# Optimization experiments

Hardware: AMD Instinct MI355X
Metric: run time of the kernel (lower is better)

The kernel has to match this reference:

```python
import jax, jax.numpy as jnp
import numpy as np

N = 50000          # nodes
E = 400000         # edges
MUL = 32           # multiplicity per irrep
NUM_NEIGHBORS = 8.0
INV_SQRT3 = 1.0 / np.sqrt(3.0)  # w3j(1,1,0) coefficient


def setup_inputs() -> dict:
    key = jax.random.key(0)
    ks = jax.random.split(key, 20)
    inp = {
        # node_input: 32x0e (dim 32) + 32x1o (dim 96) = 128
        "node_input": jax.random.normal(ks[0], (N, 4 * MUL), jnp.float32),
        "node_attr": jnp.ones((N, 1), jnp.float32),           # 1x0e trivial attr
        "edge_src": jax.random.randint(ks[1], (E,), 0, N, jnp.int32),
        "edge_dst": jax.random.randint(ks[2], (E,), 0, N, jnp.int32),
        "edge_attr": jax.random.normal(ks[3], (E, 4), jnp.float32),   # 1x0e + 1x1o
        "edge_scalars": jax.random.normal(ks[4], (E, 16), jnp.float32),
        # FullyConnectedTensorProduct weights (uvw, node_attr has mul 1)
        "w_sc0": jax.random.normal(ks[5], (MUL, MUL), jnp.float32),
        "w_sc1": jax.random.normal(ks[6], (MUL, MUL), jnp.float32),
        "w_lin1_0": jax.random.normal(ks[7], (MUL, MUL), jnp.float32),
        "w_lin1_1": jax.random.normal(ks[8], (MUL, MUL), jnp.float32),
        # radial FC net -> per-edge TP weights (numel = 4*MUL = 128)
        "fc_w1": jax.random.normal(ks[9], (16, 64), jnp.float32),
        "fc_w2": jax.random.normal(ks[10], (64, 4 * MUL), jnp.float32),
        # lin2: irreps_mid (64x0e+64x1o) x attr -> output
        "w_lin2_0": jax.random.normal(ks[11], (2 * MUL, MUL), jnp.float32),
        "w_lin2_1": jax.random.normal(ks[12], (2 * MUL, MUL), jnp.float32),
        # alpha: irreps_mid x attr -> 0e (zero-init in original; small randn for a nontrivial test)
        "w_alpha": 0.1 * jax.random.normal(ks[13], (2 * MUL, 1), jnp.float32),
        # sc_edges: irreps_mid x edge_attr -> edge_attr
        "w_se0a": jax.random.normal(ks[14], (2 * MUL,), jnp.float32),  # mid0e x ea0e -> 0e
        "w_se0b": jax.random.normal(ks[15], (2 * MUL,), jnp.float32),  # mid1o x ea1o -> 0e
        "w_se1a": jax.random.normal(ks[16], (2 * MUL,), jnp.float32),  # mid0e x ea1o -> 1o
        "w_se1b": jax.random.normal(ks[17], (2 * MUL,), jnp.float32),  # mid1o x ea0e -> 1o
    }
    return inp


def reference(node_input, node_attr, edge_src, edge_dst, edge_attr, edge_scalars,
              w_sc0, w_sc1, w_lin1_0, w_lin1_1, fc_w1, fc_w2,
              w_lin2_0, w_lin2_1, w_alpha, w_se0a, w_se0b, w_se1a, w_se1b):
    inv_nn = 1.0 / jnp.sqrt(jnp.asarray(NUM_NEIGHBORS, node_input.dtype))
    n = node_input.shape[0]
    x0 = node_input[:, :MUL]                       # (N, 32)   32x0e
    x1 = node_input[:, MUL:].reshape(n, MUL, 3)    # (N, 32, 3) 32x1o
    a = node_attr                                  # (N, 1)
    s_in = 1.0 / np.sqrt(MUL)                      # FCTP fan-in normalization

    # self-connection: FCTP(input, attr) -> output
    sc0 = (x0 @ w_sc0) * a * s_in
    sc1 = jnp.einsum('num,uw->nwm', x1, w_sc1) * a[:, :, None] * s_in
    node_self = jnp.concatenate([sc0, sc1.reshape(n, 3 * MUL)], axis=1)  # (N, 128)

    # lin1: FCTP(input, attr) -> input irreps
    f0 = (x0 @ w_lin1_0) * a * s_in
    f1 = jnp.einsum('num,uw->nwm', x1, w_lin1_1) * a[:, :, None] * s_in

    # gather source node features per edge
    g0 = f0[edge_src]                              # (E, 32)
    g1 = f1[edge_src]                              # (E, 32, 3)
    ea0 = edge_attr[:, :1]                         # (E, 1)   1x0e
    ea1 = edge_attr[:, 1:]                         # (E, 3)   1x1o

    # radial net -> per-edge TP weights (FullyConnectedNet with sin activation)
    h = jnp.sin(edge_scalars @ fc_w1 * (1.0 / np.sqrt(16.0)))
    w = h @ fc_w2 * (1.0 / np.sqrt(64.0))          # (E, 128)
    wA, wB, wC, wD = jnp.split(w, 4, axis=1)       # each (E, 32)

    # uvu tensor product, 4 instructions
    mA = wA * g0 * ea0                                           # 0e x 0e -> 0e
    mD = wD * jnp.einsum('eum,em->eu', g1, ea1) * INV_SQRT3      # 1o x 1o -> 0e
    mB = (wB * g0)[:, :, None] * ea1[:, None, :]                 # 0e x 1o -> 1o
    mC = (wC[:, :, None] * g1) * ea0[:, :, None]                 # 1o x 0e -> 1o
    mid0 = jnp.concatenate([mA, mD], axis=1)       # (E, 64)  64x0e
    mid1 = jnp.concatenate([mB, mC], axis=1)       # (E, 64, 3) 64x1o

    # scatter-add to destination nodes
    n0 = jax.ops.segment_sum(mid0, edge_dst, num_segments=n) * inv_nn
    n1 = jax.ops.segment_sum(mid1, edge_dst, num_segments=n) * inv_nn

    s_mid = 1.0 / np.sqrt(2 * MUL)
    out0 = (n0 @ w_lin2_0) * a * s_mid
    out1 = jnp.einsum('num,uw->nwm', n1, w_lin2_1) * a[:, :, None] * s_mid
    node_conv = jnp.concatenate([out0, out1.reshape(n, 3 * MUL)], axis=1)

    # alpha gate (sc.output_mask is all ones here, so alpha = 1 - 1 + alpha*1)
    alpha = (n0 @ w_alpha) * a * s_mid             # (N, 1)
    node_conv_out = node_self + alpha * node_conv  # (N, 128)

    # sc_edges: FCTP(mid, edge_attr) -> edge_attr irreps; fan-in = 128 per output
    s_se = 1.0 / np.sqrt(4 * MUL)
    se0 = ((mid0 @ w_se0a) * ea0[:, 0]
           + jnp.einsum('eum,em,u->e', mid1, ea1, w_se0b) * INV_SQRT3) * s_se
    se1 = ((mid0 @ w_se1a)[:, None] * ea1
           + jnp.einsum('eum,u->em', mid1, w_se1b) * ea0) * s_se
    edge_conv_out = edge_attr + jnp.concatenate([se0[:, None], se1], axis=1) * inv_nn

    return node_conv_out, edge_conv_out
```

## Files before the change

### kernel.cpp

```cpp
#include <hip/hip_runtime.h>
#include <math.h>

#define N_NODES 50000
#define E_EDGES 400000
#define NPRE_BLOCKS 6250
#define NHIST_BLOCKS 1563

typedef _Float16 f16x2 __attribute__((ext_vector_type(2)));
typedef _Float16 f16x4 __attribute__((ext_vector_type(4)));
typedef _Float16 f16x8 __attribute__((ext_vector_type(8)));
typedef float    f32x4 __attribute__((ext_vector_type(4)));

static constexpr float S_IN      = 0.17677669529663687f;
static constexpr float S_MID     = 0.125f;
static constexpr float S_SE      = 0.08838834764831843f;
static constexpr float INV_NN    = 0.35355339059327373f;
static constexpr float INV_SQRT3 = 0.5773502691896258f;
static constexpr float FC1_S     = 0.25f;
static constexpr float FC2_S     = 0.125f;

__device__ inline float wave_reduce_dpp(float v) {
    int x;
    x = __builtin_amdgcn_update_dpp(0, __float_as_int(v), 0x111, 0xf, 0xf, true); v += __int_as_float(x);
    x = __builtin_amdgcn_update_dpp(0, __float_as_int(v), 0x112, 0xf, 0xf, true); v += __int_as_float(x);
    x = __builtin_amdgcn_update_dpp(0, __float_as_int(v), 0x114, 0xf, 0xf, true); v += __int_as_float(x);
    x = __builtin_amdgcn_update_dpp(0, __float_as_int(v), 0x118, 0xf, 0xf, true); v += __int_as_float(x);
    x = __builtin_amdgcn_update_dpp(0, __float_as_int(v), 0x142, 0xa, 0xf, true); v += __int_as_float(x);
    x = __builtin_amdgcn_update_dpp(0, __float_as_int(v), 0x143, 0xc, 0xf, true); v += __int_as_float(x);
    return __int_as_float(__builtin_amdgcn_readlane(__float_as_int(v), 63));
}

__global__ __launch_bounds__(256) void pre_hist_kernel(
    const float* __restrict__ node_input, const float* __restrict__ node_attr,
    const float* __restrict__ w_sc0, const float* __restrict__ w_sc1,
    const float* __restrict__ w_lin1_0, const float* __restrict__ w_lin1_1,
    float* __restrict__ out_self, float* __restrict__ ws_f,
    const int* __restrict__ edge_dst, int* __restrict__ counts)
{
    const int t = threadIdx.x;
    if (blockIdx.x >= NPRE_BLOCKS) {
        const int e = (blockIdx.x - NPRE_BLOCKS) * 256 + t;
        if (e < E_EDGES) atomicAdd(&counts[edge_dst[e]], 1);
        return;
    }
    const int n0 = blockIdx.x * 8;
    __shared__ __align__(16) float sx[8 * 128];
    __shared__ float sa[8];
    ((float4*)sx)[t] = ((const float4*)(node_input + (size_t)n0 * 128))[t];
    if (t < 8) sa[t] = node_attr[n0 + t];
    __syncthreads();

    const int half = t >> 7;
    const int idx  = t & 127;
    float wcol[32];
    int m = 0;
    if (idx < 32) {
        const float* __restrict__ W = half ? w_lin1_0 : w_sc0;
        #pragma unroll
        for (int u = 0; u < 32; ++u) wcol[u] = W[u * 32 + idx];
    } else {
        const float* __restrict__ W = half ? w_lin1_1 : w_sc1;
        const int j = idx - 32;
        const int w = j / 3; m = j % 3;
        #pragma unroll
        for (int u = 0; u < 32; ++u) wcol[u] = W[u * 32 + w];
    }
    float* __restrict__ dstp = half ? ws_f : out_self;
    #pragma unroll
    for (int k = 0; k < 8; ++k) {
        const float* x = sx + k * 128;
        float acc = 0.f;
        if (idx < 32) {
            #pragma unroll
            for (int u = 0; u < 32; ++u) acc += x[u] * wcol[u];
        } else {
            #pragma unroll
            for (int u = 0; u < 32; ++u) acc += x[32 + u * 3 + m] * wcol[u];
        }
        dstp[(size_t)(n0 + k) * 128 + idx] = acc * sa[k] * S_IN;
    }
}

__global__ __launch_bounds__(1024) void scan_block_kernel(
    const int* __restrict__ counts, int* __restrict__ cursor, int* __restrict__ bsum)
{
    __shared__ int sd[1024];
    const int t   = threadIdx.x;
    const int idx = blockIdx.x * 1024 + t;
    const int c   = (idx < N_NODES) ? counts[idx] : 0;
    sd[t] = c;
    __syncthreads();
    for (int off = 1; off < 1024; off <<= 1) {
        const int v = (t >= off) ? sd[t - off] : 0;
        __syncthreads();
        sd[t] += v;
        __syncthreads();
    }
    if (idx < N_NODES) cursor[idx] = sd[t] - c;
    if (t == 1023) bsum[blockIdx.x] = sd[1023];
}

__global__ __launch_bounds__(1024) void scan_fixup_kernel(
    int* __restrict__ cursor, const int* __restrict__ bsum)
{
    __shared__ int boff_s;
    const int t = threadIdx.x;
    if (t < 64) {
        int v = (t < (int)blockIdx.x) ? bsum[t] : 0;
        #pragma unroll
        for (int off = 32; off >= 1; off >>= 1) v += __shfl_down(v, off, 64);
        if (t == 0) boff_s = v;
    }
    __syncthreads();
    const int idx = blockIdx.x * 1024 + t;
    if (idx < N_NODES) cursor[idx] += boff_s;
}

__global__ __launch_bounds__(256) void scatter_kernel(
    const int* __restrict__ edge_dst, int* __restrict__ cursor,
    int* __restrict__ sorted_eid)
{
    const int e = blockIdx.x * 256 + threadIdx.x;
    if (e < E_EDGES) {
        const int p = atomicAdd(&cursor[edge_dst[e]], 1);
        sorted_eid[p] = e;
    }
}

__global__ __launch_bounds__(256, 4) void edge_kernel(
    const float* __restrict__ ws_f,
    const int* __restrict__ edge_src, const int* __restrict__ edge_dst,
    const float* __restrict__ edge_attr, const float* __restrict__ edge_scalars,
    const float* __restrict__ fc_w1, const float* __restrict__ fc_w2,
    const float* __restrict__ w_se0a, const float* __restrict__ w_se0b,
    const float* __restrict__ w_se1a, const float* __restrict__ w_se1b,
    const int* __restrict__ sorted_eid,
    float* __restrict__ nacc, float* __restrict__ edge_out)
{
    __shared__ __align__(16) _Float16 sArena[18944];
    __shared__ __align__(16) float sEA[64 * 4];
    __shared__ __align__(16) float sDep[4][36];
    __shared__ int sSRC[64];
    __shared__ int sDST[64];
    __shared__ int sEID[64];

    _Float16* __restrict__ sW2T  = sArena;
    _Float16* __restrict__ sHT   = sArena + 9216;
    _Float16* __restrict__ sES   = sArena + 13824;
    _Float16* __restrict__ sW1T  = sArena + 16384;
    _Float16* __restrict__ sWt   = sArena;
    _Float16* __restrict__ sMidA = sArena + 8704;
    _Float16* __restrict__ sBT   = sArena + 12928;

    const int t    = threadIdx.x;
    const int lane = t & 63;
    const int wv   = t >> 6;
    const int quad = lane >> 4;
    const int mm   = lane & 15;
    const int e0   = blockIdx.x * 64;

    {
        const int k = t >> 4, n4 = (t & 15) * 4;
        float4 v = ((const float4*)fc_w1)[t];
        sW1T[(n4 + 0) * 40 + k] = (_Float16)v.x;
        sW1T[(n4 + 1) * 40 + k] = (_Float16)v.y;
        sW1T[(n4 + 2) * 40 + k] = (_Float16)v.z;
        sW1T[(n4 + 3) * 40 + k] = (_Float16)v.w;
        const f16x4 z4 = {(_Float16)0.f, (_Float16)0.f, (_Float16)0.f, (_Float16)0.f};
        *(f16x4*)&sW1T[(t >> 2) * 40 + 16 + (t & 3) * 4] = z4;
    }
    #pragma unroll
    for (int i = 0; i < 8; ++i) {
        const int u = t + i * 256;
        const int k = u >> 5, c4 = (u & 31) * 4;
        float4 v = ((const float4*)fc_w2)[u];
        sW2T[(c4 + 0) * 72 + k] = (_Float16)v.x;
        sW2T[(c4 + 1) * 72 + k] = (_Float16)v.y;
        sW2T[(c4 + 2) * 72 + k] = (_Float16)v.z;
        sW2T[(c4 + 3) * 72 + k] = (_Float16)v.w;
    }
    {
        const int e = t >> 2, k4 = (t & 3) * 4;
        const int eid = sorted_eid[e0 + e];
        float4 v = ((const float4*)edge_scalars)[(size_t)eid * 4 + (t & 3)];
        f16x4 p = {(_Float16)v.x, (_Float16)v.y, (_Float16)v.z, (_Float16)v.w};
        *(f16x4*)&sES[e * 40 + k4] = p;
        const f16x4 z4 = {(_Float16)0.f, (_Float16)0.f, (_Float16)0.f, (_Float16)0.f};
        *(f16x4*)&sES[e * 40 + 16 + k4] = z4;
    }
    if (t < 64) {
        const int eid = sorted_eid[e0 + t];
        *(float4*)&sEA[t * 4] = ((const float4*)edge_attr)[eid];
        sEID[t] = eid;
    } else if (t < 128) {
        sSRC[t - 64] = edge_src[sorted_eid[e0 + (t - 64)]];
    } else if (t < 192) {
        sDST[t - 128] = edge_dst[sorted_eid[e0 + (t - 128)]];
    }
    __syncthreads();

    const int eb = wv * 16;

    {
        const f16x8 b_es = *(const f16x8*)&sES[(eb + mm) * 40 + quad * 8];
        #pragma unroll
        for (int jt = 0; jt < 4; ++jt) {
            const f16x8 a_w1 = *(const f16x8*)&sW1T[(jt * 16 + mm) * 40 + quad * 8];
            f32x4 d = {0.f, 0.f, 0.f, 0.f};
            d = __builtin_amdgcn_mfma_f32_16x16x32_f16(a_w1, b_es, d, 0, 0, 0);
            f16x4 hv;
            hv[0] = (_Float16)__sinf(d[0] * FC1_S);
            hv[1] = (_Float16)__sinf(d[1] * FC1_S);
            hv[2] = (_Float16)__sinf(d[2] * FC1_S);
            hv[3] = (_Float16)__sinf(d[3] * FC1_S);
            *(f16x4*)&sHT[(eb + mm) * 72 + jt * 16 + quad * 4] = hv;
        }
    }
    __syncthreads();

    f32x4 dacc[8];
    {
        const f16x8 b_lo = *(const f16x8*)&sHT[(eb + mm) * 72 + quad * 8];
        const f16x8 b_hi = *(const f16x8*)&sHT[(eb + mm) * 72 + 32 + quad * 8];
        #pragma unroll
        for (int ct = 0; ct < 8; ++ct) {
            const f16x8 a_lo = *(const f16x8*)&sW2T[(ct * 16 + mm) * 72 + quad * 8];
            const f16x8 a_hi = *(const f16x8*)&sW2T[(ct * 16 + mm) * 72 + 32 + quad * 8];
            f32x4 d = {0.f, 0.f, 0.f, 0.f};
            d = __builtin_amdgcn_mfma_f32_16x16x32_f16(a_lo, b_lo, d, 0, 0, 0);
            d = __builtin_amdgcn_mfma_f32_16x16x32_f16(a_hi, b_hi, d, 0, 0, 0);
            dacc[ct] = d;
        }
    }
    __syncthreads();

    {
        #pragma unroll
        for (int ct = 0; ct < 8; ++ct) {
            f16x4 v;
            v[0] = (_Float16)(dacc[ct][0] * FC2_S);
            v[1] = (_Float16)(dacc[ct][1] * FC2_S);
            v[2] = (_Float16)(dacc[ct][2] * FC2_S);
            v[3] = (_Float16)(dacc[ct][3] * FC2_S);
            *(f16x4*)&sWt[(eb + mm) * 136 + ct * 16 + quad * 4] = v;
        }
        const f16x8 z8 = {};
        for (int i = t; i < 528; i += 256) *(f16x8*)&sBT[i * 8] = z8;
    }
    __syncthreads();
    {
        const int u = t & 63, p = t >> 6;
        const float ev = (p == 0) ? w_se0a[u] : w_se1b[u];
        const float ov = (p == 0) ? w_se1a[u] : w_se0b[u];
        sBT[(2 * p) * 264 + 4 * u + p]     = (_Float16)ev;
        sBT[(2 * p + 1) * 264 + 4 * u + p] = (_Float16)ov;
    }
    __syncthreads();

    const bool hi = lane >= 32;
    const int  u  = lane - 32;
    const int idxA = hi ? (32 + 3 * u) : lane;
    const int idxB = hi ? (33 + 3 * u) : lane;
    const int idxC = hi ? (34 + 3 * u) : lane;
    const int col1 = hi ? (96 + u) : lane;
    const int col2 = hi ? (64 + u) : (32 + lane);

    int   cur = -1;
    float am0 = 0.f, axx = 0.f, ayy = 0.f, azz = 0.f;
    _Float16* __restrict__ myA = sMidA + wv * 1056;
    const _Float16* __restrict__ arow = myA + (mm & 3) * 264;
    const _Float16* __restrict__ brow = sBT + mm * 264;

    for (int b = 0; b < 4; ++b) {
        float ga[4], gb[4], gc[4];
        #pragma unroll
        for (int i = 0; i < 4; ++i) {
            const int el = eb + b * 4 + i;
            const float* fr = ws_f + (size_t)sSRC[el] * 128;
            ga[i] = fr[idxA]; gb[i] = fr[idxB]; gc[i] = fr[idxC];
        }
        #pragma unroll
        for (int i = 0; i < 4; ++i) {
            const int el  = eb + b * 4 + i;
            const int dst = sDST[el];
            const float ea0 = sEA[el * 4 + 0];
            const float e1x = sEA[el * 4 + 1];
            const float e1y = sEA[el * 4 + 2];
            const float e1z = sEA[el * 4 + 3];
            const float w1v = (float)sWt[el * 136 + col1];
            const float w2v = (float)sWt[el * 136 + col2];

            float mid0, m1x, m1y, m1z;
            if (!hi) {
                mid0 = w1v * ga[i] * ea0;
                const float wbg = w2v * ga[i];
                m1x = wbg * e1x; m1y = wbg * e1y; m1z = wbg * e1z;
            } else {
                const float dot = ga[i] * e1x + gb[i] * e1y + gc[i] * e1z;
                mid0 = w1v * dot * INV_SQRT3;
                const float wce = w2v * ea0;
                m1x = wce * ga[i]; m1y = wce * gb[i]; m1z = wce * gc[i];
            }

            if (dst != cur) {
                if (cur >= 0) {
                    float* np_ = nacc + (size_t)cur * 256;
                    atomicAdd(np_ + lane, am0);
                    atomicAdd(np_ + 64 + lane * 3 + 0, axx);
                    atomicAdd(np_ + 64 + lane * 3 + 1, ayy);
                    atomicAdd(np_ + 64 + lane * 3 + 2, azz);
                }
                cur = dst; am0 = axx = ayy = azz = 0.f;
            }
            am0 += mid0; axx += m1x; ayy += m1y; azz += m1z;

            f16x4 mv;
            mv[0] = (_Float16)mid0; mv[1] = (_Float16)m1x;
            mv[2] = (_Float16)m1y;  mv[3] = (_Float16)m1z;
            *(f16x4*)&myA[i * 264 + 4 * lane] = mv;
        }

        f32x4 d = {0.f, 0.f, 0.f, 0.f};
        #pragma unroll
        for (int ks = 0; ks < 8; ++ks) {
            const f16x8 a  = *(const f16x8*)&arow[ks * 32 + quad * 8];
            const f16x8 bb = *(const f16x8*)&brow[ks * 32 + quad * 8];
            d = __builtin_amdgcn_mfma_f32_16x16x32_f16(a, bb, d, 0, 0, 0);
        }
        if (lane < 8) {
            float4 f4; f4.x = d[0]; f4.y = d[1]; f4.z = d[2]; f4.w = d[3];
            *(float4*)&sDep[wv][lane * 4] = f4;
        }
        if (lane < 4) {
            const int el = eb + b * 4 + lane;
            const float c0 = sDep[wv][ 0 + lane], c1 = sDep[wv][ 4 + lane];
            const float c2 = sDep[wv][ 8 + lane], c3 = sDep[wv][12 + lane];
            const float c4 = sDep[wv][16 + lane], c5 = sDep[wv][20 + lane];
            const float c6 = sDep[wv][24 + lane], c7 = sDep[wv][28 + lane];
            const float ea0 = sEA[el * 4 + 0];
            const float e1x = sEA[el * 4 + 1];
            const float e1y = sEA[el * 4 + 2];
            const float e1z = sEA[el * 4 + 3];
            const float s0 = c0 * ea0 + (c3 * e1x + c5 * e1y + c7 * e1z) * INV_SQRT3;
            float4 o;
            o.x = ea0 + s0 * S_SE * INV_NN;
            o.y = e1x + (c1 * e1x + c2 * ea0) * S_SE * INV_NN;
            o.z = e1y + (c1 * e1y + c4 * ea0) * S_SE * INV_NN;
            o.w = e1z + (c1 * e1z + c6 * ea0) * S_SE * INV_NN;
            *(float4*)&edge_out[(size_t)sEID[el] * 4] = o;
        }
    }
    if (cur >= 0) {
        float* np_ = nacc + (size_t)cur * 256;
        atomicAdd(np_ + lane, am0);
        atomicAdd(np_ + 64 + lane * 3 + 0, axx);
        atomicAdd(np_ + 64 + lane * 3 + 1, ayy);
        atomicAdd(np_ + 64 + lane * 3 + 2, azz);
    }
}

__global__ __launch_bounds__(128) void node_post_kernel(
    const float* __restrict__ nacc, const float* __restrict__ node_attr,
    const float* __restrict__ w_lin2_0, const float* __restrict__ w_lin2_1,
    const float* __restrict__ w_alpha, float* __restrict__ out)
{
    const int n0 = blockIdx.x * 8, t = threadIdx.x;
    __shared__ __align__(16) float sn[8 * 256];
    __shared__ float salpha[8];
    const float4* src = (const float4*)(nacc + (size_t)n0 * 256);
    #pragma unroll
    for (int i = 0; i < 4; ++i) ((float4*)sn)[t + i * 128] = src[t + i * 128];
    __syncthreads();

    if (t < 64) {
        const float wa = w_alpha[t];
        #pragma unroll
        for (int k = 0; k < 8; ++k) {
            const float r = wave_reduce_dpp(sn[k * 256 + t] * wa);
            if (t == 0) salpha[k] = r;
        }
    }
    __syncthreads();

    float wcol[64];
    int m = 0;
    if (t < 32) {
        #pragma unroll
        for (int u = 0; u < 64; ++u) wcol[u] = w_lin2_0[u * 32 + t];
    } else {
        const int j = t - 32; const int w = j / 3; m = j % 3;
        #pragma unroll
        for (int u = 0; u < 64; ++u) wcol[u] = w_lin2_1[u * 32 + w];
    }
    #pragma unroll
    for (int k = 0; k < 8; ++k) {
        const float* s = sn + k * 256;
        float acc = 0.f;
        if (t < 32) {
            #pragma unroll
            for (int u = 0; u < 64; ++u) acc += s[u] * wcol[u];
        } else {
            #pragma unroll
            for (int u = 0; u < 64; ++u) acc += s[64 + u * 3 + m] * wcol[u];
        }
        const float a  = node_attr[n0 + k];
        const float sc = a * S_MID * INV_NN;
        const size_t o = (size_t)(n0 + k) * 128 + t;
        out[o] = out[o] + (salpha[k] * sc) * (acc * sc);
    }
}

extern "C" void kernel_launch(void* const* d_in, const int* in_sizes, int n_in,
                              void* d_out, int out_size, void* d_ws, size_t ws_size,
                              hipStream_t stream)
{
    const float* node_input   = (const float*)d_in[0];
    const float* node_attr    = (const float*)d_in[1];
    const int*   edge_src     = (const int*)d_in[2];
    const int*   edge_dst     = (const int*)d_in[3];
    const float* edge_attr    = (const float*)d_in[4];
    const float* edge_scalars = (const float*)d_in[5];
    const float* w_sc0        = (const float*)d_in[6];
    const float* w_sc1        = (const float*)d_in[7];
    const float* w_lin1_0     = (const float*)d_in[8];
    const float* w_lin1_1     = (const float*)d_in[9];
    const float* fc_w1        = (const float*)d_in[10];
    const float* fc_w2        = (const float*)d_in[11];
    const float* w_lin2_0     = (const float*)d_in[12];
    const float* w_lin2_1     = (const float*)d_in[13];
    const float* w_alpha      = (const float*)d_in[14];
    const float* w_se0a       = (const float*)d_in[15];
    const float* w_se0b       = (const float*)d_in[16];
    const float* w_se1a       = (const float*)d_in[17];
    const float* w_se1b       = (const float*)d_in[18];

    float* out      = (float*)d_out;
    float* edge_out = out + (size_t)N_NODES * 128;

    float* ws_f   = (float*)d_ws;
    float* nacc   = ws_f + (size_t)N_NODES * 128;
    int*   counts = (int*)(nacc + (size_t)N_NODES * 256);
    int*   cursor = counts + N_NODES;
    int*   sid    = cursor + N_NODES;
    int*   bsum   = sid + E_EDGES;

    hipMemsetAsync(nacc, 0,
        ((size_t)N_NODES * 256 + N_NODES) * sizeof(float), stream);

    pre_hist_kernel<<<NPRE_BLOCKS + NHIST_BLOCKS, 256, 0, stream>>>(
        node_input, node_attr, w_sc0, w_sc1, w_lin1_0, w_lin1_1, out, ws_f,
        edge_dst, counts);

    scan_block_kernel<<<49, 1024, 0, stream>>>(counts, cursor, bsum);
    scan_fixup_kernel<<<49, 1024, 0, stream>>>(cursor, bsum);
    scatter_kernel<<<(E_EDGES + 255) / 256, 256, 0, stream>>>(edge_dst, cursor, sid);

    edge_kernel<<<E_EDGES / 64, 256, 0, stream>>>(
        ws_f, edge_src, edge_dst, edge_attr, edge_scalars, fc_w1, fc_w2,
        w_se0a, w_se0b, w_se1a, w_se1b, sid, nacc, edge_out);

    node_post_kernel<<<N_NODES / 8, 128, 0, stream>>>(
        nacc, node_attr, w_lin2_0, w_lin2_1, w_alpha, out);
}
```

Before: 414.3 us.

## Load FC1 operands into registers, prefetch gathers early, shrink LDS for occupancy

Result: no change. 420.9 us (+1.6%).

```diff
diff --git a/kernel.cpp b/kernel.cpp
--- a/kernel.cpp
+++ b/kernel.cpp
@@ -18,6 +18,8 @@
 static constexpr float INV_SQRT3 = 0.5773502691896258f;
 static constexpr float FC1_S     = 0.25f;
 static constexpr float FC2_S     = 0.125f;
+
+#define BAR_LDS() asm volatile("s_waitcnt lgkmcnt(0)\n\ts_barrier" ::: "memory")
 
 __device__ inline float wave_reduce_dpp(float v) {
     int x;
@@ -127,7 +129,7 @@
     }
 }
 
-__global__ __launch_bounds__(256, 4) void edge_kernel(
+__global__ __launch_bounds__(256, 5) void edge_kernel(
     const float* __restrict__ ws_f,
     const int* __restrict__ edge_src, const int* __restrict__ edge_dst,
     const float* __restrict__ edge_attr, const float* __restrict__ edge_scalars,
@@ -137,7 +139,7 @@
     const int* __restrict__ sorted_eid,
     float* __restrict__ nacc, float* __restrict__ edge_out)
 {
-    __shared__ __align__(16) _Float16 sArena[18944];
+    __shared__ __align__(16) _Float16 sArena[15040];
     __shared__ __align__(16) float sEA[64 * 4];
     __shared__ __align__(16) float sDep[4][36];
     __shared__ int sSRC[64];
@@ -146,8 +148,6 @@
 
     _Float16* __restrict__ sW2T  = sArena;
     _Float16* __restrict__ sHT   = sArena + 9216;
-    _Float16* __restrict__ sES   = sArena + 13824;
-    _Float16* __restrict__ sW1T  = sArena + 16384;
     _Float16* __restrict__ sWt   = sArena;
     _Float16* __restrict__ sMidA = sArena + 8704;
     _Float16* __restrict__ sBT   = sArena + 12928;
@@ -158,17 +158,31 @@
     const int quad = lane >> 4;
     const int mm   = lane & 15;
     const int e0   = blockIdx.x * 64;
-
-    {
-        const int k = t >> 4, n4 = (t & 15) * 4;
-        float4 v = ((const float4*)fc_w1)[t];
-        sW1T[(n4 + 0) * 40 + k] = (_Float16)v.x;
-        sW1T[(n4 + 1) * 40 + k] = (_Float16)v.y;
-        sW1T[(n4 + 2) * 40 + k] = (_Float16)v.z;
-        sW1T[(n4 + 3) * 40 + k] = (_Float16)v.w;
-        const f16x4 z4 = {(_Float16)0.f, (_Float16)0.f, (_Float16)0.f, (_Float16)0.f};
-        *(f16x4*)&sW1T[(t >> 2) * 40 + 16 + (t & 3) * 4] = z4;
-    }
+    const int eb   = wv * 16;
+
+    f16x8 a_w1[4];
+    f16x8 b_es = {};
+    if (quad < 2) {
+        const int myeid = sorted_eid[e0 + eb + mm];
+        const float4* esp = (const float4*)edge_scalars + (size_t)myeid * 4 + quad * 2;
+        const float4 v0 = esp[0];
+        const float4 v1 = esp[1];
+        b_es[0] = (_Float16)v0.x; b_es[1] = (_Float16)v0.y;
+        b_es[2] = (_Float16)v0.z; b_es[3] = (_Float16)v0.w;
+        b_es[4] = (_Float16)v1.x; b_es[5] = (_Float16)v1.y;
+        b_es[6] = (_Float16)v1.z; b_es[7] = (_Float16)v1.w;
+        const float* wb = fc_w1 + (quad << 3) * 64 + mm;
+        #pragma unroll
+        for (int jt = 0; jt < 4; ++jt) {
+            #pragma unroll
+            for (int s = 0; s < 8; ++s)
+                a_w1[jt][s] = (_Float16)wb[s * 64 + jt * 16];
+        }
+    } else {
+        #pragma unroll
+        for (int jt = 0; jt < 4; ++jt) a_w1[jt] = (f16x8){};
+    }
+
     #pragma unroll
     for (int i = 0; i < 8; ++i) {
         const int u = t + i * 256;
@@ -179,15 +193,6 @@
         sW2T[(c4 + 2) * 72 + k] = (_Float16)v.z;
         sW2T[(c4 + 3) * 72 + k] = (_Float16)v.w;
     }
-    {
-        const int e = t >> 2, k4 = (t & 3) * 4;
-        const int eid = sorted_eid[e0 + e];
-        float4 v = ((const float4*)edge_scalars)[(size_t)eid * 4 + (t & 3)];
-        f16x4 p = {(_Float16)v.x, (_Float16)v.y, (_Float16)v.z, (_Float16)v.w};
-        *(f16x4*)&sES[e * 40 + k4] = p;
-        const f16x4 z4 = {(_Float16)0.f, (_Float16)0.f, (_Float16)0.f, (_Float16)0.f};
-        *(f16x4*)&sES[e * 40 + 16 + k4] = z4;
-    }
     if (t < 64) {
         const int eid = sorted_eid[e0 + t];
         *(float4*)&sEA[t * 4] = ((const float4*)edge_attr)[eid];
@@ -197,26 +202,35 @@
     } else if (t < 192) {
         sDST[t - 128] = edge_dst[sorted_eid[e0 + (t - 128)]];
     }
-    __syncthreads();
-
-    const int eb = wv * 16;
-
-    {
-        const f16x8 b_es = *(const f16x8*)&sES[(eb + mm) * 40 + quad * 8];
-        #pragma unroll
-        for (int jt = 0; jt < 4; ++jt) {
-            const f16x8 a_w1 = *(const f16x8*)&sW1T[(jt * 16 + mm) * 40 + quad * 8];
-            f32x4 d = {0.f, 0.f, 0.f, 0.f};
-            d = __builtin_amdgcn_mfma_f32_16x16x32_f16(a_w1, b_es, d, 0, 0, 0);
-            f16x4 hv;
-            hv[0] = (_Float16)__sinf(d[0] * FC1_S);
-            hv[1] = (_Float16)__sinf(d[1] * FC1_S);
-            hv[2] = (_Float16)__sinf(d[2] * FC1_S);
-            hv[3] = (_Float16)__sinf(d[3] * FC1_S);
-            *(f16x4*)&sHT[(eb + mm) * 72 + jt * 16 + quad * 4] = hv;
-        }
-    }
-    __syncthreads();
+    BAR_LDS();
+
+    const bool hi = lane >= 32;
+    const int  u  = lane - 32;
+    const int idxA = hi ? (32 + 3 * u) : lane;
+    const int idxB = hi ? (33 + 3 * u) : lane;
+    const int idxC = hi ? (34 + 3 * u) : lane;
+    const int col1 = hi ? (96 + u) : lane;
+    const int col2 = hi ? (64 + u) : (32 + lane);
+
+    float ga[4][4], gb[4][4], gc[4][4];
+    #pragma unroll
+    for (int i = 0; i < 4; ++i) {
+        const float* fr = ws_f + (size_t)sSRC[eb + i] * 128;
+        ga[0][i] = fr[idxA]; gb[0][i] = fr[idxB]; gc[0][i] = fr[idxC];
+    }
+
+    #pragma unroll
+    for (int jt = 0; jt < 4; ++jt) {
+        f32x4 d = {0.f, 0.f, 0.f, 0.f};
+        d = __builtin_amdgcn_mfma_f32_16x16x32_f16(a_w1[jt], b_es, d, 0, 0, 0);
+        f16x4 hv;
+        hv[0] = (_Float16)__sinf(d[0] * FC1_S);
+        hv[1] = (_Float16)__sinf(d[1] * FC1_S);
+        hv[2] = (_Float16)__sinf(d[2] * FC1_S);
+        hv[3] = (_Float16)__sinf(d[3] * FC1_S);
+        *(f16x4*)&sHT[(eb + mm) * 72 + jt * 16 + quad * 4] = hv;
+    }
+    BAR_LDS();
 
     f32x4 dacc[8];
     {
@@ -232,7 +246,7 @@
             dacc[ct] = d;
         }
     }
-    __syncthreads();
+    BAR_LDS();
 
     {
         #pragma unroll
@@ -245,39 +259,32 @@
             *(f16x4*)&sWt[(eb + mm) * 136 + ct * 16 + quad * 4] = v;
         }
         const f16x8 z8 = {};
-        for (int i = t; i < 528; i += 256) *(f16x8*)&sBT[i * 8] = z8;
-    }
-    __syncthreads();
+        for (int i = t; i < 264; i += 256) *(f16x8*)&sBT[i * 8] = z8;
+    }
+    BAR_LDS();
     {
-        const int u = t & 63, p = t >> 6;
-        const float ev = (p == 0) ? w_se0a[u] : w_se1b[u];
-        const float ov = (p == 0) ? w_se1a[u] : w_se0b[u];
-        sBT[(2 * p) * 264 + 4 * u + p]     = (_Float16)ev;
-        sBT[(2 * p + 1) * 264 + 4 * u + p] = (_Float16)ov;
-    }
-    __syncthreads();
-
-    const bool hi = lane >= 32;
-    const int  u  = lane - 32;
-    const int idxA = hi ? (32 + 3 * u) : lane;
-    const int idxB = hi ? (33 + 3 * u) : lane;
-    const int idxC = hi ? (34 + 3 * u) : lane;
-    const int col1 = hi ? (96 + u) : lane;
-    const int col2 = hi ? (64 + u) : (32 + lane);
+        const int uu = t & 63, p = t >> 6;
+        const float ev = (p == 0) ? w_se0a[uu] : w_se1b[uu];
+        const float ov = (p == 0) ? w_se1a[uu] : w_se0b[uu];
+        sBT[(2 * p) * 264 + 4 * uu + p]     = (_Float16)ev;
+        sBT[(2 * p + 1) * 264 + 4 * uu + p] = (_Float16)ov;
+    }
+    BAR_LDS();
 
     int   cur = -1;
     float am0 = 0.f, axx = 0.f, ayy = 0.f, azz = 0.f;
     _Float16* __restrict__ myA = sMidA + wv * 1056;
     const _Float16* __restrict__ arow = myA + (mm & 3) * 264;
-    const _Float16* __restrict__ brow = sBT + mm * 264;
-
+    const _Float16* __restrict__ brow = sBT + (mm & 7) * 264;
+
+    #pragma unroll
     for (int b = 0; b < 4; ++b) {
-        float ga[4], gb[4], gc[4];
-        #pragma unroll
-        for (int i = 0; i < 4; ++i) {
-            const int el = eb + b * 4 + i;
-            const float* fr = ws_f + (size_t)sSRC[el] * 128;
-            ga[i] = fr[idxA]; gb[i] = fr[idxB]; gc[i] = fr[idxC];
+        if (b < 3) {
+            #pragma unroll
+            for (int i = 0; i < 4; ++i) {
+                const float* fr = ws_f + (size_t)sSRC[eb + (b + 1) * 4 + i] * 128;
+                ga[b + 1][i] = fr[idxA]; gb[b + 1][i] = fr[idxB]; gc[b + 1][i] = fr[idxC];
+            }
         }
         #pragma unroll
         for (int i = 0; i < 4; ++i) {
@@ -292,14 +299,14 @@
 
             float mid0, m1x, m1y, m1z;
             if (!hi) {
-                mid0 = w1v * ga[i] * ea0;
-                const float wbg = w2v * ga[i];
+                mid0 = w1v * ga[b][i] * ea0;
+                const float wbg = w2v * ga[b][i];
                 m1x = wbg * e1x; m1y = wbg * e1y; m1z = wbg * e1z;
             } else {
-                const float dot = ga[i] * e1x + gb[i] * e1y + gc[i] * e1z;
+                const float dot = ga[b][i] * e1x + gb[b][i] * e1y + gc[b][i] * e1z;
                 mid0 = w1v * dot * INV_SQRT3;
                 const float wce = w2v * ea0;
-                m1x = wce * ga[i]; m1y = wce * gb[i]; m1z = wce * gc[i];
+                m1x = wce * ga[b][i]; m1y = wce * gb[b][i]; m1z = wce * gc[b][i];
             }
 
             if (dst != cur) {
```
